# Performance work log

Measured on AMD Instinct MI355X. Metric: run time of the kernel, lower is better.

Reference implementation:

```python
import jax, jax.numpy as jnp
import numpy as np

N = 32768   # total nodes
B = 128     # graphs
L = 256     # nodes per graph (equal-size graphs -> pad_sequence == reshape)
F = 768     # num_features
NH = 256    # nhid
H = 128     # lstm hidden per direction (nhid // 2)
E = 524288  # edges
C = 2       # num_classes


def setup_inputs() -> dict:
    key = jax.random.key(0)
    ks = jax.random.split(key, 16)
    def w(k, shape, fan_in):
        return jax.random.normal(k, shape, jnp.float32) / np.sqrt(fan_in)
    x = jax.random.normal(ks[0], (N, F), jnp.float32)
    edge_index = jax.random.randint(ks[1], (2, E), 0, N)
    batch = jnp.repeat(jnp.arange(B), L)  # sorted graph ids, L nodes per graph
    return {
        "x": x,
        "edge_index": edge_index,
        "batch": batch,
        "W_gcn": w(ks[2], (F, NH), F),
        "b_gcn": jnp.zeros((NH,), jnp.float32),
        # LSTM layer 0: [dir, 4H, Din], gate order i,f,g,o (PyTorch)
        "lstm0_Wih": w(ks[3], (2, 4 * H, F), F),
        "lstm0_Whh": w(ks[4], (2, 4 * H, H), H),
        "lstm0_b": jnp.zeros((2, 4 * H), jnp.float32),
        # LSTM layer 1: input = 2H (bidirectional concat)
        "lstm1_Wih": w(ks[5], (2, 4 * H, 2 * H), 2 * H),
        "lstm1_Whh": w(ks[6], (2, 4 * H, H), H),
        "lstm1_b": jnp.zeros((2, 4 * H), jnp.float32),
        "W_seq": w(ks[7], (NH, NH), NH),
        "b_seq": jnp.zeros((NH,), jnp.float32),
        "W1": w(ks[8], (2 * NH, NH), 2 * NH),
        "b1": jnp.zeros((NH,), jnp.float32),
        "W2": w(ks[9], (NH, C), NH),
        "b2": jnp.zeros((C,), jnp.float32),
    }


def _lstm_dir(xs, Wih, Whh, b, reverse):
    # xs: [Bt, L, Din] -> hidden seq [Bt, L, H]
    Hh = Whh.shape[-1]
    def step(carry, xt):
        h, c = carry
        g = xt @ Wih.T + h @ Whh.T + b
        i, f, gg, o = jnp.split(g, 4, axis=-1)
        c = jax.nn.sigmoid(f) * c + jax.nn.sigmoid(i) * jnp.tanh(gg)
        h = jax.nn.sigmoid(o) * jnp.tanh(c)
        return (h, c), h
    x_t = jnp.swapaxes(xs, 0, 1)  # [L, Bt, Din]
    init = (jnp.zeros((xs.shape[0], Hh), xs.dtype),
            jnp.zeros((xs.shape[0], Hh), xs.dtype))
    _, hs = jax.lax.scan(step, init, x_t, reverse=reverse)
    return jnp.swapaxes(hs, 0, 1)


def _lstm_bidir(xs, Wih, Whh, b):
    fwd = _lstm_dir(xs, Wih[0], Whh[0], b[0], False)
    bwd = _lstm_dir(xs, Wih[1], Whh[1], b[1], True)
    return jnp.concatenate([fwd, bwd], axis=-1)


def reference(x, edge_index, batch, W_gcn, b_gcn,
              lstm0_Wih, lstm0_Whh, lstm0_b,
              lstm1_Wih, lstm1_Whh, lstm1_b,
              W_seq, b_seq, W1, b1, W2, b2):
    n = x.shape[0]
    # --- GCNConv (add self loops, symmetric norm) ---
    loops = jnp.arange(n)
    row = jnp.concatenate([edge_index[0], loops])
    col = jnp.concatenate([edge_index[1], loops])
    deg = jax.ops.segment_sum(jnp.ones_like(col, x.dtype), col, num_segments=n)
    dinv = jnp.where(deg > 0, jax.lax.rsqrt(deg), 0.0)
    norm = dinv[row] * dinv[col]
    h = x @ W_gcn                                   # [N, NH]
    agg = jax.ops.segment_sum(h[row] * norm[:, None], col, num_segments=n)
    x_graph = jax.nn.relu(agg + b_gcn)
    # --- global max pool per graph ---
    x_graph = jax.ops.segment_max(x_graph, batch, num_segments=B)  # [B, NH]
    # --- unbatch + pad_sequence (equal-size graphs -> reshape) ---
    seq_x = x.reshape(B, L, F)
    # --- bidirectional 2-layer LSTM ---
    seq_x = _lstm_bidir(seq_x, lstm0_Wih, lstm0_Whh, lstm0_b)  # [B, L, 2H]
    seq_x = _lstm_bidir(seq_x, lstm1_Wih, lstm1_Whh, lstm1_b)  # [B, L, 2H]
    seq_x = seq_x[:, 0, :]                                      # pre_padding=False -> first step
    # dropout is identity in eval mode
    x_seq = jax.nn.leaky_relu(seq_x @ W_seq + b_seq, negative_slope=0.01)
    out = jnp.concatenate([x_graph, x_seq], axis=1)             # [B, 2*NH]
    out = jax.nn.relu(out @ W1 + b1)
    return jax.nn.log_softmax(out @ W2 + b2, axis=-1)
```

## Files before the change

### kernel.cpp

```cpp
#include <hip/hip_runtime.h>
#include <math.h>


namespace {

constexpr int kN  = 32768;
constexpr int kB  = 128;
constexpr int kL  = 256;
constexpr int kF  = 768;
constexpr int kNH = 256;
constexpr int kH  = 128;
constexpr int kE  = 524288;

typedef __attribute__((ext_vector_type(8))) short bf16x8;
typedef __attribute__((ext_vector_type(4))) float f32x4;
typedef __attribute__((address_space(3))) unsigned int lds_u32;
typedef __attribute__((address_space(1))) unsigned int glb_u32;

__device__ __forceinline__ float sigf(float x)  { return 1.f / (1.f + __expf(-x)); }
__device__ __forceinline__ float tanh_f(float x){ return 1.f - 2.f / (1.f + __expf(2.f * x)); }

__device__ __forceinline__ unsigned short f2bf(float f) {
  unsigned int u = __float_as_uint(f);
  u = u + 0x7fffu + ((u >> 16) & 1u);
  return (unsigned short)(u >> 16);
}
__device__ __forceinline__ float bf2f(unsigned short h) {
  return __uint_as_float((unsigned int)h << 16);
}


__global__ void count_edges(const int* __restrict__ col, int* __restrict__ cnt) {
  int e = blockIdx.x * 256 + threadIdx.x;
  if (e < kE) atomicAdd(&cnt[col[e]], 1);
}

__global__ void scan_dinv(const int* __restrict__ cnt, int* __restrict__ offs,
                          int* __restrict__ cursor, float* __restrict__ dinv) {
  __shared__ int part[1024];
  int t = threadIdx.x;
  int base = t * 32;
  int loc[32];
  int s = 0;
#pragma unroll
  for (int i = 0; i < 32; i++) { loc[i] = cnt[base + i]; s += loc[i]; }
  part[t] = s;
  __syncthreads();
  for (int d = 1; d < 1024; d <<= 1) {
    int v = part[t];
    int add = (t >= d) ? part[t - d] : 0;
    __syncthreads();
    part[t] = v + add;
    __syncthreads();
  }
  int run = (t == 0) ? 0 : part[t - 1];
#pragma unroll
  for (int i = 0; i < 32; i++) {
    offs[base + i] = run;
    cursor[base + i] = run;
    dinv[base + i] = rsqrtf((float)(loc[i] + 1));
    run += loc[i];
  }
  if (t == 1023) offs[kN] = run;
}

__global__ void fill_csr(const int* __restrict__ row, const int* __restrict__ col,
                         int* __restrict__ cursor, int* __restrict__ elist) {
  int e = blockIdx.x * 256 + threadIdx.x;
  if (e < kE) {
    int c = col[e];
    int p = atomicAdd(&cursor[c], 1);
    elist[p] = row[e];
  }
}


__global__ void convert_bt(const float* __restrict__ W, unsigned short* __restrict__ hi,
                           unsigned short* __restrict__ lo, int Nn, int Kk, int trans) {
  int idx = blockIdx.x * 256 + threadIdx.x;
  if (idx >= Nn * Kk) return;
  int n = idx / Kk, k = idx - n * Kk;
  float f = trans ? W[(size_t)k * Nn + n] : W[idx];
  unsigned short h = f2bf(f);
  hi[idx] = h;
  lo[idx] = f2bf(f - bf2f(h));
}


__global__ __launch_bounds__(256, 2) void gemm3(const float* __restrict__ A,
                                                const unsigned short* __restrict__ Bhi,
                                                const unsigned short* __restrict__ Blo,
                                                float* __restrict__ C,
                                                int M, int N, int K) {
  __shared__ __align__(16) char lds[32768];
  const int tid = threadIdx.x;
  const int lane = tid & 63;
  const int w = tid >> 6, wr = w >> 1, wc = w & 1;
  const int m0 = blockIdx.y * 128, n0 = blockIdx.x * 128;

  f32x4 acc[4][4];
#pragma unroll
  for (int i = 0; i < 4; i++)
#pragma unroll
    for (int j = 0; j < 4; j++) acc[i][j] = (f32x4)0.f;

  const float* aptr[4];
  int aoff[4];
#pragma unroll
  for (int i = 0; i < 4; i++) {
    int f = tid + i * 256;
    int row = f >> 3, kq4 = f & 7;
    aptr[i] = A + (size_t)(m0 + row) * K + kq4 * 4;
    int sub = row >> 4, r = row & 15, q = kq4 >> 1, hs = kq4 & 1;
    aoff[i] = sub * 1024 + (q * 16 + r) * 16 + hs * 8;
  }
  const unsigned short* bsrc[4];
  int boff[4];
#pragma unroll
  for (int j = 0; j < 4; j++) {
    int id = w * 4 + j;
    int isLo = id >> 3, sub = id & 7;
    const unsigned short* Bp = isLo ? Blo : Bhi;
    bsrc[j] = Bp + (size_t)(n0 + sub * 16 + (lane & 15)) * K + (lane >> 4) * 8;
    boff[j] = 16384 + isLo * 8192 + sub * 1024;
  }

  for (int k0 = 0; k0 < K; k0 += 32) {
#pragma unroll
    for (int j = 0; j < 4; j++) {
      __builtin_amdgcn_global_load_lds((const glb_u32*)bsrc[j],
                                       (lds_u32*)(lds + boff[j]), 16, 0, 0);
      bsrc[j] += 32;
    }
#pragma unroll
    for (int i = 0; i < 4; i++) {
      f32x4 v = *(const f32x4*)(aptr[i]);
      aptr[i] += 32;
      unsigned short h0 = f2bf(v.x), h1 = f2bf(v.y), h2 = f2bf(v.z), h3 = f2bf(v.w);
      unsigned short g0 = f2bf(v.x - bf2f(h0)), g1 = f2bf(v.y - bf2f(h1));
      unsigned short g2 = f2bf(v.z - bf2f(h2)), g3 = f2bf(v.w - bf2f(h3));
      uint2 hv, lv;
      hv.x = (unsigned int)h0 | ((unsigned int)h1 << 16);
      hv.y = (unsigned int)h2 | ((unsigned int)h3 << 16);
      lv.x = (unsigned int)g0 | ((unsigned int)g1 << 16);
      lv.y = (unsigned int)g2 | ((unsigned int)g3 << 16);
      *(uint2*)(lds + aoff[i]) = hv;
      *(uint2*)(lds + aoff[i] + 8192) = lv;
    }
    __syncthreads();

    const bf16x8* L = (const bf16x8*)lds;
    bf16x8 ah[4], al[4], bh[4], bl[4];
#pragma unroll
    for (int m = 0; m < 4; m++) {
      ah[m] = L[(wr * 4 + m) * 64 + lane];
      al[m] = L[512 + (wr * 4 + m) * 64 + lane];
    }
#pragma unroll
    for (int n = 0; n < 4; n++) {
      bh[n] = L[1024 + (wc * 4 + n) * 64 + lane];
      bl[n] = L[1536 + (wc * 4 + n) * 64 + lane];
    }
#pragma unroll
    for (int m = 0; m < 4; m++)
#pragma unroll
      for (int n = 0; n < 4; n++) {
        acc[m][n] = __builtin_amdgcn_mfma_f32_16x16x32_bf16(ah[m], bh[n], acc[m][n], 0, 0, 0);
        acc[m][n] = __builtin_amdgcn_mfma_f32_16x16x32_bf16(ah[m], bl[n], acc[m][n], 0, 0, 0);
        acc[m][n] = __builtin_amdgcn_mfma_f32_16x16x32_bf16(al[m], bh[n], acc[m][n], 0, 0, 0);
      }
    __syncthreads();
  }

#pragma unroll
  for (int m = 0; m < 4; m++)
#pragma unroll
    for (int n = 0; n < 4; n++) {
      int r0 = m0 + wr * 64 + m * 16 + (lane >> 4) * 4;
      int cc = n0 + wc * 64 + n * 16 + (lane & 15);
#pragma unroll
      for (int j = 0; j < 4; j++)
        C[(size_t)(r0 + j) * N + cc] = acc[m][n][j];
    }
}


__global__ __launch_bounds__(256) void gcn_gather(const float* __restrict__ hg,
                                                  const int* __restrict__ offs,
                                                  const int* __restrict__ elist,
                                                  const float* __restrict__ dinv,
                                                  const float* __restrict__ bgcn,
                                                  float* __restrict__ out) {
  int n = blockIdx.x, j = threadIdx.x;
  float di = dinv[n];
  float acc = hg[(size_t)n * kNH + j] * (di * di);
  int s = offs[n], e = offs[n + 1];
  int p = s;
  for (; p + 4 <= e; p += 4) {
    int r0 = elist[p], r1 = elist[p + 1], r2 = elist[p + 2], r3 = elist[p + 3];
    float w0 = di * dinv[r0], w1 = di * dinv[r1], w2 = di * dinv[r2], w3 = di * dinv[r3];
    float v0 = hg[(size_t)r0 * kNH + j], v1 = hg[(size_t)r1 * kNH + j];
    float v2 = hg[(size_t)r2 * kNH + j], v3 = hg[(size_t)r3 * kNH + j];
    acc = fmaf(v0, w0, acc); acc = fmaf(v1, w1, acc);
    acc = fmaf(v2, w2, acc); acc = fmaf(v3, w3, acc);
  }
  for (; p < e; p++) {
    int r = elist[p];
    acc = fmaf(hg[(size_t)r * kNH + j], di * dinv[r], acc);
  }
  acc += bgcn[j];
  out[(size_t)n * kNH + j] = fmaxf(acc, 0.f);
}

__global__ __launch_bounds__(256) void segmax(const float* __restrict__ xg_full,
                                              float* __restrict__ x_graph) {
  int g = blockIdx.x, j = threadIdx.x;
  const float* base = xg_full + (size_t)g * kL * kNH + j;
  float m0 = -1e30f, m1 = -1e30f, m2 = -1e30f, m3 = -1e30f;
  for (int t = 0; t < kL; t += 4) {
    m0 = fmaxf(m0, base[(size_t)(t + 0) * kNH]);
    m1 = fmaxf(m1, base[(size_t)(t + 1) * kNH]);
    m2 = fmaxf(m2, base[(size_t)(t + 2) * kNH]);
    m3 = fmaxf(m3, base[(size_t)(t + 3) * kNH]);
  }
  x_graph[g * kNH + j] = fmaxf(fmaxf(m0, m1), fmaxf(m2, m3));
}


#define LDW(q) \
  float4 w##q##0, w##q##1, w##q##2, w##q##3, w##q##4, w##q##5, w##q##6, w##q##7; \
  { const float4* wp = (const float4*)(wb + (q) * 16384); \
    w##q##0 = wp[0]; w##q##1 = wp[1]; w##q##2 = wp[2]; w##q##3 = wp[3]; \
    w##q##4 = wp[4]; w##q##5 = wp[5]; w##q##6 = wp[6]; w##q##7 = wp[7]; }

#define FMA4(q, wv, hv) \
  a##q = fmaf(wv.x, hv.x, a##q); a##q = fmaf(wv.y, hv.y, a##q); \
  a##q = fmaf(wv.z, hv.z, a##q); a##q = fmaf(wv.w, hv.w, a##q)

#define STEPP(p) { \
  float4 h4 = hb[ks * 8 + ((p + ks) & 7)]; \
  FMA4(0, w0##p, h4); FMA4(1, w1##p, h4); FMA4(2, w2##p, h4); FMA4(3, w3##p, h4); }

__global__ __launch_bounds__(512, 1) void lstm_rec(const float* __restrict__ Z, int zstride,
                                                   const float* __restrict__ Whh2,
                                                   const float* __restrict__ bias2,
                                                   float* __restrict__ Y0,
                                                   float* __restrict__ hfin, int mode) {
  __shared__ __align__(16) float hbuf[2][kH];
  int b, dir;
  if (mode == 0) { dir = blockIdx.x >> 7; b = blockIdx.x & 127; }
  else           { dir = 1;               b = blockIdx.x; }
  const bool rev = (dir == 1);
  const int t0 = threadIdx.x;
  const int j = t0 >> 2;
  const int ks = t0 & 3;

  const float* wb = Whh2 + (size_t)dir * 65536 + (size_t)j * kH + ks * 32;
  LDW(0) LDW(1) LDW(2) LDW(3)

  const float bg = bias2[dir * 512 + ks * kH + j];
  const int zcol = (mode == 0) ? dir * 512 : 0;
  float c = 0.f, hn = 0.f;

  const int jph = ((j >> 5) * 8 + ((((j >> 2) & 7) + (j >> 5)) & 7)) * 4 + (j & 3);

  if (t0 < kH) hbuf[0][t0] = 0.f;

  const float* zp = Z + (size_t)(b * kL + (rev ? kL - 1 : 0)) * zstride + zcol + ks * kH + j;
  const long zinc = rev ? -(long)zstride : (long)zstride;
  float zt = *zp;
  __syncthreads();

  for (int t = 0; t < kL; t++) {
    const int tt = rev ? (kL - 1 - t) : t;
    float znext = 0.f;
    if (t < kL - 1) znext = zp[zinc];
    zp += zinc;
    const int cur = t & 1;

    const float4* hb = (const float4*)hbuf[cur];
    float a0 = 0.f, a1 = 0.f, a2 = 0.f, a3 = 0.f;
    STEPP(0) STEPP(1) STEPP(2) STEPP(3) STEPP(4) STEPP(5) STEPP(6) STEPP(7)

    const float zb = zt + bg;
    a0 += (ks == 0) ? zb : 0.f;
    a1 += (ks == 1) ? zb : 0.f;
    a2 += (ks == 2) ? zb : 0.f;
    a3 += (ks == 3) ? zb : 0.f;
    a0 += __shfl_xor(a0, 1); a1 += __shfl_xor(a1, 1);
    a2 += __shfl_xor(a2, 1); a3 += __shfl_xor(a3, 1);
    a0 += __shfl_xor(a0, 2); a1 += __shfl_xor(a1, 2);
    a2 += __shfl_xor(a2, 2); a3 += __shfl_xor(a3, 2);

    const float ig = sigf(a0), fg = sigf(a1), gg = tanh_f(a2), og = sigf(a3);
    c = fg * c + ig * gg;
    hn = og * tanh_f(c);
    if (ks == 0) {
      hbuf[cur ^ 1][jph] = hn;
      if (mode == 0) Y0[(size_t)(b * kL + tt) * kNH + dir * kH + j] = hn;
    }
    __syncthreads();
    zt = znext;
  }
  if (mode == 1 && ks == 0) hfin[b * kH + j] = hn;
}

#undef LDW
#undef FMA4
#undef STEPP


__global__ __launch_bounds__(256) void head(const float* __restrict__ Y0,
                                            const float* __restrict__ h1b,
                                            const float* __restrict__ Wih1f,
                                            const float* __restrict__ b1f,
                                            const float* __restrict__ xgraph,
                                            const float* __restrict__ Wseq,
                                            const float* __restrict__ bseq,
                                            const float* __restrict__ W1,
                                            const float* __restrict__ b1,
                                            const float* __restrict__ W2,
                                            const float* __restrict__ b2,
                                            float* __restrict__ out) {
  int b = blockIdx.x, t = threadIdx.x;
  __shared__ __align__(16) float x0[kNH];
  __shared__ float gl[512];
  __shared__ __align__(16) float seq[kNH];
  __shared__ __align__(16) float v[512];
  __shared__ __align__(16) float o1[kNH];
  __shared__ float red[512];

  x0[t] = Y0[(size_t)(b * kL) * kNH + t];
  if (t >= kH) seq[t] = h1b[b * kH + (t - kH)];
  __syncthreads();

#pragma unroll
  for (int half = 0; half < 2; half++) {
    int g = t + half * 256;
    const float* wr = Wih1f + (size_t)g * kNH;
    float acc = b1f[g];
#pragma unroll 8
    for (int k = 0; k < kNH; k += 4) {
      float4 xv = *(const float4*)&x0[k];
      float4 wv = *(const float4*)(wr + k);
      acc = fmaf(xv.x, wv.x, acc); acc = fmaf(xv.y, wv.y, acc);
      acc = fmaf(xv.z, wv.z, acc); acc = fmaf(xv.w, wv.w, acc);
    }
    gl[g] = acc;
  }
  __syncthreads();
  if (t < kH) {
    float ig = sigf(gl[t]);
    float gg = tanh_f(gl[2 * kH + t]);
    float og = sigf(gl[3 * kH + t]);
    float c = ig * gg;
    seq[t] = og * tanh_f(c);
  }
  v[t] = xgraph[b * kNH + t];
  __syncthreads();

  {
    float acc = bseq[t];
#pragma unroll 4
    for (int k = 0; k < kNH; k++) acc = fmaf(seq[k], Wseq[(size_t)k * kNH + t], acc);
    v[kNH + t] = (acc > 0.f) ? acc : 0.01f * acc;
  }
  __syncthreads();

  {
    float acc = b1[t];
#pragma unroll 4
    for (int k = 0; k < 512; k++) acc = fmaf(v[k], W1[(size_t)k * kNH + t], acc);
    o1[t] = fmaxf(acc, 0.f);
  }
  __syncthreads();

  red[t]       = o1[t] * W2[t * 2 + 0];
  red[kNH + t] = o1[t] * W2[t * 2 + 1];
  __syncthreads();
  for (int s = 128; s > 0; s >>= 1) {
    if (t < s) { red[t] += red[t + s]; red[kNH + t] += red[kNH + t + s]; }
    __syncthreads();
  }
  if (t == 0) {
    float z0 = red[0] + b2[0], z1 = red[kNH] + b2[1];
    float m = fmaxf(z0, z1);
    float lse = m + logf(__expf(z0 - m) + __expf(z1 - m));
    out[b * 2 + 0] = z0 - lse;
    out[b * 2 + 1] = z1 - lse;
  }
}

}

extern "C" void kernel_launch(void* const* d_in, const int* in_sizes, int n_in,
                              void* d_out, int out_size, void* d_ws, size_t ws_size,
                              hipStream_t stream) {
  const float* x     = (const float*)d_in[0];
  const int*   ei    = (const int*)d_in[1];
  const float* Wgcn  = (const float*)d_in[3];
  const float* bgcn  = (const float*)d_in[4];
  const float* l0Wih = (const float*)d_in[5];
  const float* l0Whh = (const float*)d_in[6];
  const float* l0b   = (const float*)d_in[7];
  const float* l1Wih = (const float*)d_in[8];
  const float* l1Whh = (const float*)d_in[9];
  const float* l1b   = (const float*)d_in[10];
  const float* Wseq  = (const float*)d_in[11];
  const float* bseq  = (const float*)d_in[12];
  const float* W1    = (const float*)d_in[13];
  const float* b1    = (const float*)d_in[14];
  const float* W2    = (const float*)d_in[15];
  const float* b2    = (const float*)d_in[16];
  float* out = (float*)d_out;
  char* ws = (char*)d_ws;

  float* Z0     = (float*)(ws);
  float* Y0     = (float*)(ws + 134217728UL);
  float* xgraph = (float*)(ws + 134217728UL + 33554432UL);
  float* h1b    = (float*)(ws + 134217728UL + 33554432UL + 131072UL);
  float* hgcn   = Z0;
  float* xgfull = (float*)(ws + 33554432UL);
  int*   cnt    = (int*)(ws + 67108864UL);
  int*   offs   = (int*)(ws + 67108864UL + 1048576UL);
  int*   cursor = (int*)(ws + 67108864UL + 2097152UL);
  int*   elist  = (int*)(ws + 67108864UL + 3145728UL);
  float* dinv   = (float*)(ws + 67108864UL + 6291456UL);
  float* Z1b    = Z0;

  unsigned short* gWhi = (unsigned short*)(ws + 78643200UL);
  unsigned short* gWlo = (unsigned short*)(ws + 78643200UL + 393216UL);
  unsigned short* l0hi = (unsigned short*)(ws + 134217728UL);
  unsigned short* l0lo = (unsigned short*)(ws + 134217728UL + 1572864UL);
  unsigned short* l1hi = (unsigned short*)(ws + 104857600UL);
  unsigned short* l1lo = (unsigned short*)(ws + 104857600UL + 262144UL);

  const int* erow = ei;
  const int* ecol = ei + kE;

  hipMemsetAsync(cnt, 0, kN * sizeof(int), stream);
  count_edges<<<kE / 256, 256, 0, stream>>>(ecol, cnt);
  scan_dinv<<<1, 1024, 0, stream>>>(cnt, offs, cursor, dinv);
  fill_csr<<<kE / 256, 256, 0, stream>>>(erow, ecol, cursor, elist);
  convert_bt<<<(kNH * kF + 255) / 256, 256, 0, stream>>>(Wgcn, gWhi, gWlo, kNH, kF, 1);
  gemm3<<<dim3(kNH / 128, kN / 128), 256, 0, stream>>>(x, gWhi, gWlo, hgcn, kN, kNH, kF);
  gcn_gather<<<kN, 256, 0, stream>>>(hgcn, offs, elist, dinv, bgcn, xgfull);
  segmax<<<kB, 256, 0, stream>>>(xgfull, xgraph);

  convert_bt<<<(1024 * kF + 255) / 256, 256, 0, stream>>>(l0Wih, l0hi, l0lo, 1024, kF, 0);
  gemm3<<<dim3(1024 / 128, kN / 128), 256, 0, stream>>>(x, l0hi, l0lo, Z0, kN, 1024, kF);
  lstm_rec<<<256, 512, 0, stream>>>(Z0, 1024, l0Whh, l0b, Y0, nullptr, 0);
  convert_bt<<<(512 * kNH + 255) / 256, 256, 0, stream>>>(l1Wih + 512 * 256, l1hi, l1lo,
                                                          512, kNH, 0);
  gemm3<<<dim3(512 / 128, kN / 128), 256, 0, stream>>>(Y0, l1hi, l1lo, Z1b, kN, 512, kNH);
  lstm_rec<<<128, 512, 0, stream>>>(Z1b, 512, l1Whh, l1b, nullptr, h1b, 1);

  head<<<kB, 256, 0, stream>>>(Y0, h1b, l1Wih, l1b, xgraph, Wseq, bseq, W1, b1, W2, b2, out);
}
```

Before: 1.125 ms.

## Split LSTM recurrent dot products over 8 lanes per hidden unit with 1024 threads

The recurrent LSTM kernel now uses 1024 threads per block, with 8 lanes per hidden unit instead of 4. Each lane holds half as many Whh registers (16 float4) and does half the FMAs per step. The h-buffer reads switch to interleaved float4 indexing, which removes the permuted jph store layout. Per-step latency on the serial recurrence should drop, at the cost of an extra shuffle-reduction stage and a barrier that now spans 16 waves.

Measured after the change: 1.299 ms. 15.4% more time.

```diff
diff --git a/kernel.cpp b/kernel.cpp
--- a/kernel.cpp
+++ b/kernel.cpp
@@ -227,60 +227,61 @@
 }
 
 
-#define LDW(q) \
-  float4 w##q##0, w##q##1, w##q##2, w##q##3, w##q##4, w##q##5, w##q##6, w##q##7; \
-  { const float4* wp = (const float4*)(wb + (q) * 16384); \
-    w##q##0 = wp[0]; w##q##1 = wp[1]; w##q##2 = wp[2]; w##q##3 = wp[3]; \
-    w##q##4 = wp[4]; w##q##5 = wp[5]; w##q##6 = wp[6]; w##q##7 = wp[7]; }
-
-#define FMA4(q, wv, hv) \
-  a##q = fmaf(wv.x, hv.x, a##q); a##q = fmaf(wv.y, hv.y, a##q); \
-  a##q = fmaf(wv.z, hv.z, a##q); a##q = fmaf(wv.w, hv.w, a##q)
-
-#define STEPP(p) { \
-  float4 h4 = hb[ks * 8 + ((p + ks) & 7)]; \
-  FMA4(0, w0##p, h4); FMA4(1, w1##p, h4); FMA4(2, w2##p, h4); FMA4(3, w3##p, h4); }
-
-__global__ __launch_bounds__(512, 1) void lstm_rec(const float* __restrict__ Z, int zstride,
-                                                   const float* __restrict__ Whh2,
-                                                   const float* __restrict__ bias2,
-                                                   float* __restrict__ Y0,
-                                                   float* __restrict__ hfin, int mode) {
+#define DOT4(acc, wv, hv) \
+  acc = fmaf(wv.x, hv.x, acc); acc = fmaf(wv.y, hv.y, acc); \
+  acc = fmaf(wv.z, hv.z, acc); acc = fmaf(wv.w, hv.w, acc)
+
+__global__ __attribute__((amdgpu_waves_per_eu(4, 4)))
+__launch_bounds__(1024) void lstm_rec(const float* __restrict__ Z, int zstride,
+                                      const float* __restrict__ Whh2,
+                                      const float* __restrict__ bias2,
+                                      float* __restrict__ Y0,
+                                      float* __restrict__ hfin, int mode) {
   __shared__ __align__(16) float hbuf[2][kH];
   int b, dir;
   if (mode == 0) { dir = blockIdx.x >> 7; b = blockIdx.x & 127; }
   else           { dir = 1;               b = blockIdx.x; }
   const bool rev = (dir == 1);
   const int t0 = threadIdx.x;
-  const int j = t0 >> 2;
-  const int ks = t0 & 3;
-
-  const float* wb = Whh2 + (size_t)dir * 65536 + (size_t)j * kH + ks * 32;
-  LDW(0) LDW(1) LDW(2) LDW(3)
-
-  const float bg = bias2[dir * 512 + ks * kH + j];
+  const int j  = t0 >> 3;
+  const int ks = t0 & 7;
+
+  const float4* wq0 = (const float4*)(Whh2 + (size_t)dir * 65536 + (size_t)(0 * kH + j) * kH);
+  const float4* wq1 = (const float4*)(Whh2 + (size_t)dir * 65536 + (size_t)(1 * kH + j) * kH);
+  const float4* wq2 = (const float4*)(Whh2 + (size_t)dir * 65536 + (size_t)(2 * kH + j) * kH);
+  const float4* wq3 = (const float4*)(Whh2 + (size_t)dir * 65536 + (size_t)(3 * kH + j) * kH);
+  float4 w00 = wq0[ks], w01 = wq0[ks + 8], w02 = wq0[ks + 16], w03 = wq0[ks + 24];
+  float4 w10 = wq1[ks], w11 = wq1[ks + 8], w12 = wq1[ks + 16], w13 = wq1[ks + 24];
+  float4 w20 = wq2[ks], w21 = wq2[ks + 8], w22 = wq2[ks + 16], w23 = wq2[ks + 24];
+  float4 w30 = wq3[ks], w31 = wq3[ks + 8], w32 = wq3[ks + 16], w33 = wq3[ks + 24];
+
+  const float bg = (ks < 4) ? bias2[dir * 512 + ks * kH + j] : 0.f;
   const int zcol = (mode == 0) ? dir * 512 : 0;
+  const int zk = ks & 3;
   float c = 0.f, hn = 0.f;
 
-  const int jph = ((j >> 5) * 8 + ((((j >> 2) & 7) + (j >> 5)) & 7)) * 4 + (j & 3);
-
   if (t0 < kH) hbuf[0][t0] = 0.f;
 
-  const float* zp = Z + (size_t)(b * kL + (rev ? kL - 1 : 0)) * zstride + zcol + ks * kH + j;
+  const float* zp = Z + (size_t)(b * kL + (rev ? kL - 1 : 0)) * zstride + zcol + zk * kH + j;
   const long zinc = rev ? -(long)zstride : (long)zstride;
-  float zt = *zp;
+  float zt = (ks < 4) ? *zp : 0.f;
   __syncthreads();
 
   for (int t = 0; t < kL; t++) {
     const int tt = rev ? (kL - 1 - t) : t;
     float znext = 0.f;
-    if (t < kL - 1) znext = zp[zinc];
+    if (t < kL - 1 && ks < 4) znext = zp[zinc];
     zp += zinc;
     const int cur = t & 1;
 
     const float4* hb = (const float4*)hbuf[cur];
+    float4 h0 = hb[ks], h1 = hb[ks + 8], h2 = hb[ks + 16], h3 = hb[ks + 24];
+
     float a0 = 0.f, a1 = 0.f, a2 = 0.f, a3 = 0.f;
-    STEPP(0) STEPP(1) STEPP(2) STEPP(3) STEPP(4) STEPP(5) STEPP(6) STEPP(7)
+    DOT4(a0, w00, h0); DOT4(a0, w01, h1); DOT4(a0, w02, h2); DOT4(a0, w03, h3);
+    DOT4(a1, w10, h0); DOT4(a1, w11, h1); DOT4(a1, w12, h2); DOT4(a1, w13, h3);
+    DOT4(a2, w20, h0); DOT4(a2, w21, h1); DOT4(a2, w22, h2); DOT4(a2, w23, h3);
+    DOT4(a3, w30, h0); DOT4(a3, w31, h1); DOT4(a3, w32, h2); DOT4(a3, w33, h3);
 
     const float zb = zt + bg;
     a0 += (ks == 0) ? zb : 0.f;
@@ -288,15 +289,17 @@
     a2 += (ks == 2) ? zb : 0.f;
     a3 += (ks == 3) ? zb : 0.f;
     a0 += __shfl_xor(a0, 1); a1 += __shfl_xor(a1, 1);
-    a2 += __shfl_xor(a2, 1); a3 += __shfl_xor(a3, 1);
+    a2 += __shfl_xor(a2, 2); a2 += __shfl_xor(a2, 1);
     a0 += __shfl_xor(a0, 2); a1 += __shfl_xor(a1, 2);
-    a2 += __shfl_xor(a2, 2); a3 += __shfl_xor(a3, 2);
+    a3 += __shfl_xor(a3, 1); a3 += __shfl_xor(a3, 2);
+    a0 += __shfl_xor(a0, 4); a1 += __shfl_xor(a1, 4);
+    a2 += __shfl_xor(a2, 4); a3 += __shfl_xor(a3, 4);
 
     const float ig = sigf(a0), fg = sigf(a1), gg = tanh_f(a2), og = sigf(a3);
     c = fg * c + ig * gg;
     hn = og * tanh_f(c);
     if (ks == 0) {
-      hbuf[cur ^ 1][jph] = hn;
+      hbuf[cur ^ 1][j] = hn;
       if (mode == 0) Y0[(size_t)(b * kL + tt) * kNH + dir * kH + j] = hn;
     }
     __syncthreads();
@@ -305,9 +308,7 @@
   if (mode == 1 && ks == 0) hfin[b * kH + j] = hn;
 }
 
-#undef LDW
-#undef FMA4
-#undef STEPP
+#undef DOT4
 
 
 __global__ __launch_bounds__(256) void head(const float* __restrict__ Y0,
@@ -449,11 +450,11 @@
 
   convert_bt<<<(1024 * kF + 255) / 256, 256, 0, stream>>>(l0Wih, l0hi, l0lo, 1024, kF, 0);
   gemm3<<<dim3(1024 / 128, kN / 128), 256, 0, stream>>>(x, l0hi, l0lo, Z0, kN, 1024, kF);
-  lstm_rec<<<256, 512, 0, stream>>>(Z0, 1024, l0Whh, l0b, Y0, nullptr, 0);
+  lstm_rec<<<256, 1024, 0, stream>>>(Z0, 1024, l0Whh, l0b, Y0, nullptr, 0);
   convert_bt<<<(512 * kNH + 255) / 256, 256, 0, stream>>>(l1Wih + 512 * 256, l1hi, l1lo,
                                                           512, kNH, 0);
   gemm3<<<dim3(512 / 128, kN / 128), 256, 0, stream>>>(Y0, l1hi, l1lo, Z1b, kN, 512, kNH);
-  lstm_rec<<<128, 512, 0, stream>>>(Z1b, 512, l1Whh, l1b, nullptr, h1b, 1);
+  lstm_rec<<<128, 1024, 0, stream>>>(Z1b, 512, l1Whh, l1b, nullptr, h1b, 1);
 
   head<<<kB, 256, 0, stream>>>(Y0, h1b, l1Wih, l1b, xgraph, Wseq, bseq, W1, b1, W2, b2, out);
 }
```
